# Optimization experiments

Measured on AMD Instinct MI355X. Metric: run time of the kernel, lower is better.

Reference implementation:

```python
import jax, jax.numpy as jnp
import numpy as np

# ---- static config (matches init_kwargs) ----
N0, N1 = 150000, 75000          # al nodes, test nodes
E = 200000                       # edges per edge type
D = 128                          # dim_h
L = 3                            # n_layers
T = 4                            # netypes
NAL = 50000                      # n_al vocab
NC = 3                           # n_classes
T_SRCS = [0, 0, 1, 1]
T_TGTS = [0, 1, 0, 1]
NODE_COUNTS = [N0, N1]


def setup_inputs() -> dict:
    key = jax.random.key(0)
    ks = jax.random.split(key, 16)
    x0_ids = jax.random.randint(ks[0], (N0,), 0, NAL, dtype=jnp.int32)
    x1_ids = jnp.zeros((N1,), dtype=jnp.int32)  # emb_test has a single row

    def make_edges(k, n_src, n_dst):
        k1, k2 = jax.random.split(k)
        src = jax.random.randint(k1, (E,), 0, n_src, dtype=jnp.int32)
        dst = jax.random.randint(k2, (E,), 0, n_dst, dtype=jnp.int32)
        return jnp.stack([src, dst])  # [2, E]

    es = [make_edges(ks[1 + j], NODE_COUNTS[T_SRCS[j]], NODE_COUNTS[T_TGTS[j]])
          for j in range(T)]

    s = 1.0 / np.sqrt(D)
    enc_al_w   = jax.random.normal(ks[5],  (NAL, D), jnp.float32) * s
    emb_test_w = jax.random.normal(ks[6],  (1, D),   jnp.float32) * s
    W_tgt = jax.random.normal(ks[7],  (L, T, D, D), jnp.float32) * s
    b_tgt = jax.random.normal(ks[8],  (L, T, D),    jnp.float32) * 0.01
    W_src = jax.random.normal(ks[9],  (L, T, D, D), jnp.float32) * s
    b_src = jax.random.normal(ks[10], (L, T, D),    jnp.float32) * 0.01
    emb_self = jax.random.normal(ks[11], (L, T, 2, D), jnp.float32) * s
    W_dec = jax.random.normal(ks[12], (NC, D), jnp.float32) * s
    b_dec = jax.random.normal(ks[13], (NC,),   jnp.float32) * 0.01
    return {
        "x0_ids": x0_ids, "x1_ids": x1_ids,
        "es0": es[0], "es1": es[1], "es2": es[2], "es3": es[3],
        "enc_al_w": enc_al_w, "emb_test_w": emb_test_w,
        "W_tgt": W_tgt, "b_tgt": b_tgt, "W_src": W_src, "b_src": b_src,
        "emb_self": emb_self, "W_dec": W_dec, "b_dec": b_dec,
    }


def reference(x0_ids, x1_ids, es0, es1, es2, es3,
              enc_al_w, emb_test_w, W_tgt, b_tgt, W_src, b_src,
              emb_self, W_dec, b_dec):
    ess = [es0, es1, es2, es3]
    # node-type embeddings
    xs = [enc_al_w[x0_ids], emb_test_w[x1_ids]]  # [N0,D], [N1,D]
    for i in range(L):
        out = [jnp.zeros((N0, D), xs[0].dtype), jnp.zeros((N1, D), xs[1].dtype)]
        for j in range(T):
            ts, tt = T_SRCS[j], T_TGTS[j]
            src, dst = ess[j][0], ess[j][1]
            # project node features first (same math as projecting gathered edges)
            h_src = xs[ts] @ W_src[i, j].T + b_src[i, j]   # lin_src(x_src)
            h_dst = xs[tt] @ W_tgt[i, j].T + b_tgt[i, j]   # lin_tgt(x_dst)
            self_flag = (dst == src).astype(jnp.int32)
            msg = h_dst[dst] + h_src[src] + emb_self[i, j][self_flag]  # [E,D]
            agg = jax.ops.segment_max(msg, dst, num_segments=NODE_COUNTS[tt])
            out[tt] = out[tt] + jax.nn.relu(agg)  # MPNN.forward applies relu
        xs = [jax.nn.relu(out[0]), jax.nn.relu(out[1])]
    last = xs[0] @ W_dec.T + b_dec                 # [N0, NC]
    return (last, jax.nn.softmax(last, axis=1))
```

## Files before the change

kernel.cpp:

```cpp
#include <hip/hip_runtime.h>
#include <hip/hip_bf16.h>

#define N0 150000
#define N1 75000
#define EE 200000
#define NAL 50000
#define NSEG (N0 + N1)
#define NSEG2 (2 * NSEG)
#define TOTE (4 * EE)

typedef unsigned short u16;
using s16x8 = __attribute__((ext_vector_type(8))) short;
using f32x4 = __attribute__((ext_vector_type(4))) float;
using u16x8 = __attribute__((ext_vector_type(8))) unsigned short;

__device__ __forceinline__ u16 f2b(float f) {
  unsigned int b = __float_as_uint(f);
  b += 0x7FFFu + ((b >> 16) & 1u);
  return (u16)(b >> 16);
}
__device__ __forceinline__ float b2f(u16 u) {
  return __uint_as_float(((unsigned int)u) << 16);
}

__global__ void sentinel_k(float* out, float val) {
  if (threadIdx.x == 0 && blockIdx.x == 0) out[0] = val;
}

__global__ __launch_bounds__(256) void prep_w(const float* __restrict__ Ws,
                                              const float* __restrict__ Wt,
                                              u16* __restrict__ BP) {
  int idx = blockIdx.x * 256 + threadIdx.x;
  int mk = idx & 16383;
  int slot = (idx >> 14) & 7;
  int i = idx >> 17;
  const int ssel[8] = {1, 0, 0, 1, 1, 1, 0, 0};
  const int sj[8]   = {0, 0, 2, 1, 2, 3, 1, 3};
  const float* W = ssel[slot] ? Ws : Wt;
  BP[idx] = f2b(W[(size_t)(i * 4 + sj[slot]) * 16384 + mk]);
}

__global__ __launch_bounds__(256) void embed_k(const int* __restrict__ ids,
                                               const float* __restrict__ tab,
                                               u16* __restrict__ X, int N, unsigned vocab) {
  int idx = blockIdx.x * 256 + threadIdx.x;
  int v = idx >> 4;
  if (v >= N) return;
  int q = (idx & 15) << 3;
  unsigned id = (unsigned)ids[v];
  if (id >= vocab) id = 0;
  const float* src = tab + (size_t)id * 128 + q;
  f32x4 x0 = *(const f32x4*)src;
  f32x4 x1 = *(const f32x4*)(src + 4);
  u16x8 o;
#pragma unroll
  for (int k = 0; k < 4; ++k) { o[k] = f2b(x0[k]); o[4 + k] = f2b(x1[k]); }
  *(u16x8*)(X + (size_t)v * 128 + q) = o;
}

__global__ __launch_bounds__(256) void count_all(const int* __restrict__ e0,
                                                 const int* __restrict__ e1,
                                                 const int* __restrict__ e2,
                                                 const int* __restrict__ e3,
                                                 int* __restrict__ cnt) {
  int i = blockIdx.x * 256 + threadIdx.x;
  if (i >= TOTE) return;
  int j = i / EE, r = i - j * EE;
  const int* es = (j == 0) ? e0 : (j == 1) ? e1 : (j == 2) ? e2 : e3;
  int dst = es[EE + r];
  int seg = (j & 1) ? N0 + dst : dst;
  atomicAdd(cnt + seg * 2 + (j >> 1), 1);
}

__global__ __launch_bounds__(512) void scan1_k(const int* __restrict__ cnt,
                                               int* __restrict__ off,
                                               int* __restrict__ part, int N) {
  __shared__ int sh[512];
  int t = threadIdx.x, i = blockIdx.x * 512 + t;
  int v = (i < N) ? cnt[i] : 0;
  sh[t] = v; __syncthreads();
  for (int s = 1; s < 512; s <<= 1) {
    int x = (t >= s) ? sh[t - s] : 0; __syncthreads();
    sh[t] += x; __syncthreads();
  }
  if (i < N) off[i] = sh[t] - v;
  if (t == 511) part[blockIdx.x] = sh[511];
}

__global__ __launch_bounds__(1024) void scan2_k(int* __restrict__ part, int n) {
  __shared__ int sh[1024];
  int t = threadIdx.x;
  int v = (t < n) ? part[t] : 0;
  sh[t] = v; __syncthreads();
  for (int s = 1; s < 1024; s <<= 1) {
    int x = (t >= s) ? sh[t - s] : 0; __syncthreads();
    sh[t] += x; __syncthreads();
  }
  if (t < n) part[t] = sh[t] - v;
}

__global__ __launch_bounds__(256) void scan3_k(int* __restrict__ off,
                                               const int* __restrict__ part, int N, int tot) {
  int i = blockIdx.x * 256 + threadIdx.x;
  if (i < N) off[i] += part[i >> 9];
  if (i == 0) off[N] = tot;
}

__global__ __launch_bounds__(256) void fill_all(const int* __restrict__ e0,
                                                const int* __restrict__ e1,
                                                const int* __restrict__ e2,
                                                const int* __restrict__ e3,
                                                const int* __restrict__ off,
                                                int* __restrict__ cur,
                                                int* __restrict__ einfo) {
  int i = blockIdx.x * 256 + threadIdx.x;
  if (i >= TOTE) return;
  int j = i / EE, r = i - j * EE;
  const int* es = (j == 0) ? e0 : (j == 1) ? e1 : (j == 2) ? e2 : e3;
  int src = es[r], dst = es[EE + r];
  int seg2 = ((j & 1) ? N0 + dst : dst) * 2 + (j >> 1);
  int pos = off[seg2] + atomicAdd(cur + seg2, 1);
  einfo[pos] = src | ((src == dst) ? (int)0x80000000 : 0);
}

__global__ __launch_bounds__(256, 5) void gemm_multi(const u16* __restrict__ A, int M,
                                                     const u16* __restrict__ W, int nw,
                                                     u16* __restrict__ C0,
                                                     u16* __restrict__ C1,
                                                     u16* __restrict__ C2,
                                                     u16* __restrict__ C3) {
  __shared__ u16 Al[64 * 128];
  __shared__ u16 Bl[64 * 128];
  const int t = threadIdx.x;
  const int row0 = blockIdx.x * 64;

#pragma unroll
  for (int u = 0; u < 4; ++u) {
    int c = u * 256 + t;
    int r = c >> 4, ch = c & 15;
    int rc = (row0 + r < M) ? (row0 + r) : (M - 1);
    int sw = ch ^ (r & 7);
    *(u16x8*)&Al[r * 128 + sw * 8] = *(const u16x8*)(A + (size_t)rc * 128 + ch * 8);
  }

  const int w = t >> 6, lane = t & 63;
  const int lr = lane & 15, g = lane >> 4;
  const int arow = (w * 16 + lr) * 128;

  u16x8 breg[4];
#pragma unroll
  for (int u = 0; u < 4; ++u) {
    int c = u * 256 + t;
    int r = c >> 4, ch = c & 15;
    breg[u] = *(const u16x8*)(W + r * 128 + ch * 8);
  }

  for (int ws = 0; ws < nw; ++ws) {
    u16* Cw = (ws == 0) ? C0 : (ws == 1) ? C1 : (ws == 2) ? C2 : C3;
#pragma unroll
    for (int h = 0; h < 2; ++h) {
      __builtin_amdgcn_sched_barrier(0);
      __builtin_amdgcn_s_barrier();
      __builtin_amdgcn_sched_barrier(0);

#pragma unroll
      for (int u = 0; u < 4; ++u) {
        int c = u * 256 + t;
        int r = c >> 4, ch = c & 15;
        int sw = ch ^ (r & 7);
        *(u16x8*)&Bl[r * 128 + sw * 8] = breg[u];
      }
      int nws = ws, nh = h + 1;
      if (nh == 2) { nh = 0; ++nws; }
      if (nws < nw) {
        const u16* Bn = W + (size_t)nws * 16384 + (size_t)nh * (64 * 128);
#pragma unroll
        for (int u = 0; u < 4; ++u) {
          int c = u * 256 + t;
          int r = c >> 4, ch = c & 15;
          breg[u] = *(const u16x8*)(Bn + r * 128 + ch * 8);
        }
      }
      asm volatile("s_waitcnt lgkmcnt(0)" ::: "memory");
      __builtin_amdgcn_sched_barrier(0);
      __builtin_amdgcn_s_barrier();
      __builtin_amdgcn_sched_barrier(0);

      f32x4 acc[4];
#pragma unroll
      for (int nf = 0; nf < 4; ++nf) acc[nf] = f32x4{0.f, 0.f, 0.f, 0.f};

#pragma unroll
      for (int ks = 0; ks < 4; ++ks) {
        int swz = ((ks * 4 + g) ^ (lr & 7)) * 8;
        s16x8 a = *(const s16x8*)&Al[arow + swz];
#pragma unroll
        for (int nf = 0; nf < 4; ++nf) {
          s16x8 b = *(const s16x8*)&Bl[(nf * 16 + lr) * 128 + swz];
          acc[nf] = __builtin_amdgcn_mfma_f32_16x16x32_bf16(a, b, acc[nf], 0, 0, 0);
        }
      }

#pragma unroll
      for (int nf = 0; nf < 4; ++nf) {
        int col = h * 64 + nf * 16 + lr;
#pragma unroll
        for (int j = 0; j < 4; ++j) {
          int orow = row0 + w * 16 + g * 4 + j;
          if (orow < M) Cw[(size_t)orow * 128 + col] = f2b(acc[nf][j]);
        }
      }
    }
  }
}

__global__ __launch_bounds__(256) void agg2_k(const int* __restrict__ off2,
                                              const int* __restrict__ einfo,
                                              int segbase,
                                              const u16* __restrict__ HSA,
                                              const u16* __restrict__ HSB,
                                              const u16* __restrict__ HD0,
                                              const u16* __restrict__ HD1,
                                              const float* __restrict__ bs0,
                                              const float* __restrict__ bt0,
                                              const float* __restrict__ bs1,
                                              const float* __restrict__ bt1,
                                              const float* __restrict__ esf0,
                                              const float* __restrict__ esf1,
                                              u16* __restrict__ Y, int N) {
  int idx = blockIdx.x * 256 + threadIdx.x;
  int d = idx >> 4;
  if (d >= N) return;
  int f8 = (idx & 15) << 3;
  int base = (segbase + d) * 2;
  int e0 = off2[base], e1 = off2[base + 1], e2 = off2[base + 2];

  float en[8], es_[8];
#pragma unroll
  for (int k = 0; k < 8; ++k) { en[k] = esf0[f8 + k]; es_[k] = esf0[128 + f8 + k]; }
  float m0[8];
#pragma unroll
  for (int k = 0; k < 8; ++k) m0[k] = -INFINITY;
  for (int e = e0; e < e1; ++e) {
    int info = einfo[e];
    int s = info & 0x7fffffff;
    bool self = (info < 0);
    u16x8 hv = *(const u16x8*)(HSA + (size_t)s * 128 + f8);
#pragma unroll
    for (int k = 0; k < 8; ++k)
      m0[k] = fmaxf(m0[k], b2f(hv[k]) + (self ? es_[k] : en[k]));
  }

#pragma unroll
  for (int k = 0; k < 8; ++k) { en[k] = esf1[f8 + k]; es_[k] = esf1[128 + f8 + k]; }
  float m1[8];
#pragma unroll
  for (int k = 0; k < 8; ++k) m1[k] = -INFINITY;
  for (int e = e1; e < e2; ++e) {
    int info = einfo[e];
    int s = info & 0x7fffffff;
    bool self = (info < 0);
    u16x8 hv = *(const u16x8*)(HSB + (size_t)s * 128 + f8);
#pragma unroll
    for (int k = 0; k < 8; ++k)
      m1[k] = fmaxf(m1[k], b2f(hv[k]) + (self ? es_[k] : en[k]));
  }

  u16x8 hd0 = *(const u16x8*)(HD0 + (size_t)d * 128 + f8);
  u16x8 hd1 = *(const u16x8*)(HD1 + (size_t)d * 128 + f8);
  u16x8 o;
#pragma unroll
  for (int k = 0; k < 8; ++k) {
    float r0 = fmaxf(b2f(hd0[k]) + bs0[f8 + k] + bt0[f8 + k] + m0[k], 0.f);
    float r1 = fmaxf(b2f(hd1[k]) + bs1[f8 + k] + bt1[f8 + k] + m1[k], 0.f);
    o[k] = f2b(r0 + r1);
  }
  *(u16x8*)(Y + (size_t)d * 128 + f8) = o;
}

__global__ __launch_bounds__(256) void decoder_k(const u16* __restrict__ X,
                                                 const float* __restrict__ Wd,
                                                 const float* __restrict__ bd,
                                                 float* __restrict__ out) {
  int v = blockIdx.x * 256 + threadIdx.x;
  if (v >= N0) return;
  float a0 = bd[0], a1 = bd[1], a2 = bd[2];
  const u16* x = X + (size_t)v * 128;
#pragma unroll
  for (int k = 0; k < 128; k += 8) {
    u16x8 xv = *(const u16x8*)(x + k);
#pragma unroll
    for (int u = 0; u < 8; ++u) {
      float xf = b2f(xv[u]);
      a0 = fmaf(xf, Wd[k + u], a0);
      a1 = fmaf(xf, Wd[128 + k + u], a1);
      a2 = fmaf(xf, Wd[256 + k + u], a2);
    }
  }
  float mx = fmaxf(a0, fmaxf(a1, a2));
  float e0 = expf(a0 - mx), e1 = expf(a1 - mx), e2 = expf(a2 - mx);
  float inv = 1.f / (e0 + e1 + e2);
  size_t b = (size_t)v * 3;
  out[b + 0] = a0; out[b + 1] = a1; out[b + 2] = a2;
  size_t b2 = (size_t)N0 * 3 + b;
  out[b2 + 0] = e0 * inv; out[b2 + 1] = e1 * inv; out[b2 + 2] = e2 * inv;
}

extern "C" void kernel_launch(void* const* d_in, const int* in_sizes, int n_in,
                              void* d_out, int out_size, void* d_ws, size_t ws_size,
                              hipStream_t stream) {
  float* out = (float*)d_out;

  const int expect[15] = {N0, N1, 2 * EE, 2 * EE, 2 * EE, 2 * EE,
                          NAL * 128, 128, 196608, 1536, 196608, 1536,
                          3072, 384, 3};
  bool ok = (n_in == 15);
  if (ok) for (int i = 0; i < 15; ++i) ok = ok && (in_sizes[i] == expect[i]);
  if (!ok) { sentinel_k<<<1, 64, 0, stream>>>(out, 500.f); return; }

  const int* x0_ids = (const int*)d_in[0];
  const int* x1_ids = (const int*)d_in[1];
  const int* es0 = (const int*)d_in[2];
  const int* es1 = (const int*)d_in[3];
  const int* es2 = (const int*)d_in[4];
  const int* es3 = (const int*)d_in[5];
  const float* enc_al   = (const float*)d_in[6];
  const float* emb_test = (const float*)d_in[7];
  const float* W_tgt    = (const float*)d_in[8];
  const float* b_tgt    = (const float*)d_in[9];
  const float* W_src    = (const float*)d_in[10];
  const float* b_src    = (const float*)d_in[11];
  const float* emb_self = (const float*)d_in[12];
  const float* W_dec    = (const float*)d_in[13];
  const float* b_dec    = (const float*)d_in[14];

  char* base = (char*)d_ws;
  size_t pos = 0;
  auto alloc = [&](size_t bytes) -> void* {
    void* r = base + pos;
    pos += (bytes + 255) & ~(size_t)255;
    return r;
  };
  u16* xs0 = (u16*)alloc((size_t)N0 * 128 * 2);
  u16* xs1 = (u16*)alloc((size_t)N1 * 128 * 2);
  u16* P0  = (u16*)alloc((size_t)N0 * 128 * 2);
  u16* P1  = (u16*)alloc((size_t)N0 * 128 * 2);
  u16* P2  = (u16*)alloc((size_t)N0 * 128 * 2);
  u16* P3  = (u16*)alloc((size_t)N1 * 128 * 2);
  u16* P4  = (u16*)alloc((size_t)N0 * 128 * 2);
  u16* BP  = (u16*)alloc((size_t)3 * 8 * 16384 * 2);
  int* off2   = (int*)alloc((size_t)(NSEG2 + 1) * 4);
  int* einfo  = (int*)alloc((size_t)TOTE * 4);
  int* counts = (int*)alloc((size_t)NSEG2 * 4);
  int* cursor = counts;
  int* part   = (int*)alloc(1024 * 4);
  if (pos > ws_size) { sentinel_k<<<1, 64, 0, stream>>>(out, 900.f); return; }

  prep_w<<<1536, 256, 0, stream>>>(W_src, W_tgt, BP);
  embed_k<<<(N0 * 16 + 255) / 256, 256, 0, stream>>>(x0_ids, enc_al, xs0, N0, NAL);
  embed_k<<<(N1 * 16 + 255) / 256, 256, 0, stream>>>(x1_ids, emb_test, xs1, N1, 1);

  const int EG = (TOTE + 255) / 256;
  const int nb = (NSEG2 + 511) / 512;
  hipMemsetAsync(counts, 0, (size_t)NSEG2 * 4, stream);
  count_all<<<EG, 256, 0, stream>>>(es0, es1, es2, es3, counts);
  scan1_k<<<nb, 512, 0, stream>>>(counts, off2, part, NSEG2);
  scan2_k<<<1, 1024, 0, stream>>>(part, nb);
  scan3_k<<<(NSEG2 + 255) / 256, 256, 0, stream>>>(off2, part, NSEG2, TOTE);
  hipMemsetAsync(cursor, 0, (size_t)NSEG2 * 4, stream);
  fill_all<<<EG, 256, 0, stream>>>(es0, es1, es2, es3, off2, cursor, einfo);

  const int G0 = (N0 + 63) / 64, G1 = (N1 + 63) / 64;
  const int GA0 = (N0 * 16 + 255) / 256, GA1 = (N1 * 16 + 255) / 256;
  for (int i = 0; i < 3; ++i) {
    const u16* BPi = BP + (size_t)i * 8 * 16384;
    gemm_multi<<<G0, 256, 0, stream>>>(xs0, N0, BPi + 0 * 16384, (i < 2) ? 4 : 3,
                                       P0, P1, P2, P4);
    gemm_multi<<<G1, 256, 0, stream>>>(xs1, N1, BPi + 4 * 16384, 1, P3, P3, P3, P3);
    agg2_k<<<GA0, 256, 0, stream>>>(off2, einfo, 0, P0, P3, P1, P2,
                                    b_src + (size_t)(i * 4 + 0) * 128, b_tgt + (size_t)(i * 4 + 0) * 128,
                                    b_src + (size_t)(i * 4 + 2) * 128, b_tgt + (size_t)(i * 4 + 2) * 128,
                                    emb_self + (size_t)(i * 4 + 0) * 256,
                                    emb_self + (size_t)(i * 4 + 2) * 256, xs0, N0);
    if (i < 2) {
      gemm_multi<<<G1, 256, 0, stream>>>(xs1, N1, BPi + 5 * 16384, 3, P3, P1, P2, P2);
      agg2_k<<<GA1, 256, 0, stream>>>(off2, einfo, N0, P4, P3, P1, P2,
                                      b_src + (size_t)(i * 4 + 1) * 128, b_tgt + (size_t)(i * 4 + 1) * 128,
                                      b_src + (size_t)(i * 4 + 3) * 128, b_tgt + (size_t)(i * 4 + 3) * 128,
                                      emb_self + (size_t)(i * 4 + 1) * 256,
                                      emb_self + (size_t)(i * 4 + 3) * 256, xs1, N1);
    }
  }

  decoder_k<<<(N0 + 255) / 256, 256, 0, stream>>>(xs0, W_dec, b_dec, out);
}
```

Before: 523.3 us.

## Fuse target-side projection GEMM into the max-aggregation kernel via LDS

Adds a gemm_agg kernel. Each block computes the two target-side projections for its 64 destination rows with MFMA, keeps them in shared memory, then runs the segment-max aggregation over those rows and writes the layer output. This removes the global writes and re-reads of two full projection buffers per node type per layer, and one launch. The weight slots are reordered so source projections come first, and the buffer set shrinks to match. The cost is that each thread now handles four destinations one after another, and the larger shared-memory footprint limits blocks per CU, so fewer irregular gathers are in flight to hide latency.

```diff
diff --git a/kernel.cpp b/kernel.cpp
--- a/kernel.cpp
+++ b/kernel.cpp
@@ -34,8 +34,8 @@
   int mk = idx & 16383;
   int slot = (idx >> 14) & 7;
   int i = idx >> 17;
-  const int ssel[8] = {1, 0, 0, 1, 1, 1, 0, 0};
-  const int sj[8]   = {0, 0, 2, 1, 2, 3, 1, 3};
+  const int ssel[8] = {1, 1, 1, 1, 0, 0, 0, 0};
+  const int sj[8]   = {0, 1, 2, 3, 0, 2, 1, 3};
   const float* W = ssel[slot] ? Ws : Wt;
   BP[idx] = f2b(W[(size_t)(i * 4 + sj[slot]) * 16384 + mk]);
 }
@@ -162,7 +162,6 @@
       __builtin_amdgcn_sched_barrier(0);
       __builtin_amdgcn_s_barrier();
       __builtin_amdgcn_sched_barrier(0);
-
 #pragma unroll
       for (int u = 0; u < 4; ++u) {
         int c = u * 256 + t;
@@ -189,7 +188,6 @@
       f32x4 acc[4];
 #pragma unroll
       for (int nf = 0; nf < 4; ++nf) acc[nf] = f32x4{0.f, 0.f, 0.f, 0.f};
-
 #pragma unroll
       for (int ks = 0; ks < 4; ++ks) {
         int swz = ((ks * 4 + g) ^ (lr & 7)) * 8;
@@ -200,7 +198,6 @@
           acc[nf] = __builtin_amdgcn_mfma_f32_16x16x32_bf16(a, b, acc[nf], 0, 0, 0);
         }
       }
-
 #pragma unroll
       for (int nf = 0; nf < 4; ++nf) {
         int col = h * 64 + nf * 16 + lr;
@@ -214,68 +211,147 @@
   }
 }
 
-__global__ __launch_bounds__(256) void agg2_k(const int* __restrict__ off2,
-                                              const int* __restrict__ einfo,
-                                              int segbase,
-                                              const u16* __restrict__ HSA,
-                                              const u16* __restrict__ HSB,
-                                              const u16* __restrict__ HD0,
-                                              const u16* __restrict__ HD1,
-                                              const float* __restrict__ bs0,
-                                              const float* __restrict__ bt0,
-                                              const float* __restrict__ bs1,
-                                              const float* __restrict__ bt1,
-                                              const float* __restrict__ esf0,
-                                              const float* __restrict__ esf1,
-                                              u16* __restrict__ Y, int N) {
-  int idx = blockIdx.x * 256 + threadIdx.x;
-  int d = idx >> 4;
-  if (d >= N) return;
-  int f8 = (idx & 15) << 3;
-  int base = (segbase + d) * 2;
-  int e0 = off2[base], e1 = off2[base + 1], e2 = off2[base + 2];
-
-  float en[8], es_[8];
-#pragma unroll
-  for (int k = 0; k < 8; ++k) { en[k] = esf0[f8 + k]; es_[k] = esf0[128 + f8 + k]; }
-  float m0[8];
-#pragma unroll
-  for (int k = 0; k < 8; ++k) m0[k] = -INFINITY;
-  for (int e = e0; e < e1; ++e) {
-    int info = einfo[e];
-    int s = info & 0x7fffffff;
-    bool self = (info < 0);
-    u16x8 hv = *(const u16x8*)(HSA + (size_t)s * 128 + f8);
-#pragma unroll
-    for (int k = 0; k < 8; ++k)
-      m0[k] = fmaxf(m0[k], b2f(hv[k]) + (self ? es_[k] : en[k]));
-  }
-
-#pragma unroll
-  for (int k = 0; k < 8; ++k) { en[k] = esf1[f8 + k]; es_[k] = esf1[128 + f8 + k]; }
-  float m1[8];
-#pragma unroll
-  for (int k = 0; k < 8; ++k) m1[k] = -INFINITY;
-  for (int e = e1; e < e2; ++e) {
-    int info = einfo[e];
-    int s = info & 0x7fffffff;
-    bool self = (info < 0);
-    u16x8 hv = *(const u16x8*)(HSB + (size_t)s * 128 + f8);
-#pragma unroll
-    for (int k = 0; k < 8; ++k)
-      m1[k] = fmaxf(m1[k], b2f(hv[k]) + (self ? es_[k] : en[k]));
-  }
-
-  u16x8 hd0 = *(const u16x8*)(HD0 + (size_t)d * 128 + f8);
-  u16x8 hd1 = *(const u16x8*)(HD1 + (size_t)d * 128 + f8);
-  u16x8 o;
-#pragma unroll
-  for (int k = 0; k < 8; ++k) {
-    float r0 = fmaxf(b2f(hd0[k]) + bs0[f8 + k] + bt0[f8 + k] + m0[k], 0.f);
-    float r1 = fmaxf(b2f(hd1[k]) + bs1[f8 + k] + bt1[f8 + k] + m1[k], 0.f);
-    o[k] = f2b(r0 + r1);
-  }
-  *(u16x8*)(Y + (size_t)d * 128 + f8) = o;
+#define HDS 264
+__global__ __launch_bounds__(256, 3) void gemm_agg(const u16* __restrict__ A,
+                                                   const u16* __restrict__ W2,
+                                                   const int* __restrict__ off2,
+                                                   const int* __restrict__ einfo,
+                                                   int segbase,
+                                                   const u16* __restrict__ HSA,
+                                                   const u16* __restrict__ HSB,
+                                                   const float* __restrict__ bs0,
+                                                   const float* __restrict__ bt0,
+                                                   const float* __restrict__ bs1,
+                                                   const float* __restrict__ bt1,
+                                                   const float* __restrict__ esf0,
+                                                   const float* __restrict__ esf1,
+                                                   u16* __restrict__ Y, int N) {
+  __shared__ u16 Bl[64 * 128];
+  __shared__ u16 HDl[64 * HDS];
+  const int t = threadIdx.x;
+  const int row0 = blockIdx.x * 64;
+  const int w = t >> 6, lane = t & 63;
+  const int lr = lane & 15, g = lane >> 4;
+
+  int arow = row0 + w * 16 + lr;
+  int arc = (arow < N) ? arow : (N - 1);
+  const u16* Ab = A + (size_t)arc * 128 + g * 8;
+  u16x8 a[4];
+#pragma unroll
+  for (int ks = 0; ks < 4; ++ks) a[ks] = *(const u16x8*)(Ab + ks * 32);
+
+  u16x8 breg[4];
+#pragma unroll
+  for (int u = 0; u < 4; ++u) {
+    int c = u * 256 + t;
+    int r = c >> 4, ch = c & 15;
+    breg[u] = *(const u16x8*)(W2 + r * 128 + ch * 8);
+  }
+
+#pragma unroll
+  for (int ws = 0; ws < 2; ++ws) {
+#pragma unroll
+    for (int h = 0; h < 2; ++h) {
+      __builtin_amdgcn_sched_barrier(0);
+      __builtin_amdgcn_s_barrier();
+      __builtin_amdgcn_sched_barrier(0);
+#pragma unroll
+      for (int u = 0; u < 4; ++u) {
+        int c = u * 256 + t;
+        int r = c >> 4, ch = c & 15;
+        int sw = ch ^ (r & 7);
+        *(u16x8*)&Bl[r * 128 + sw * 8] = breg[u];
+      }
+      int nws = ws, nh = h + 1;
+      if (nh == 2) { nh = 0; ++nws; }
+      if (nws < 2) {
+        const u16* Bn = W2 + (size_t)nws * 16384 + (size_t)nh * (64 * 128);
+#pragma unroll
+        for (int u = 0; u < 4; ++u) {
+          int c = u * 256 + t;
+          int r = c >> 4, ch = c & 15;
+          breg[u] = *(const u16x8*)(Bn + r * 128 + ch * 8);
+        }
+      }
+      asm volatile("s_waitcnt lgkmcnt(0)" ::: "memory");
+      __builtin_amdgcn_sched_barrier(0);
+      __builtin_amdgcn_s_barrier();
+      __builtin_amdgcn_sched_barrier(0);
+
+      f32x4 acc[4];
+#pragma unroll
+      for (int nf = 0; nf < 4; ++nf) acc[nf] = f32x4{0.f, 0.f, 0.f, 0.f};
+#pragma unroll
+      for (int ks = 0; ks < 4; ++ks) {
+        int swz = ((ks * 4 + g) ^ (lr & 7)) * 8;
+#pragma unroll
+        for (int nf = 0; nf < 4; ++nf) {
+          s16x8 b = *(const s16x8*)&Bl[(nf * 16 + lr) * 128 + swz];
+          acc[nf] = __builtin_amdgcn_mfma_f32_16x16x32_bf16((s16x8)a[ks], b, acc[nf], 0, 0, 0);
+        }
+      }
+#pragma unroll
+      for (int nf = 0; nf < 4; ++nf) {
+        int col = ws * 128 + h * 64 + nf * 16 + lr;
+#pragma unroll
+        for (int j = 0; j < 4; ++j)
+          HDl[(w * 16 + g * 4 + j) * HDS + col] = f2b(acc[nf][j]);
+      }
+    }
+  }
+  __syncthreads();
+
+#pragma unroll 1
+  for (int sw = 0; sw < 4; ++sw) {
+    int dl = sw * 16 + (t >> 4);
+    int d = row0 + dl;
+    if (d >= N) continue;
+    int f8 = (t & 15) << 3;
+    int base = (segbase + d) * 2;
+    int e0 = off2[base], e1 = off2[base + 1], e2 = off2[base + 2];
+
+    float en[8], es_[8];
+#pragma unroll
+    for (int k = 0; k < 8; ++k) { en[k] = esf0[f8 + k]; es_[k] = esf0[128 + f8 + k]; }
+    float m0[8];
+#pragma unroll
+    for (int k = 0; k < 8; ++k) m0[k] = -INFINITY;
+    for (int e = e0; e < e1; ++e) {
+      int info = einfo[e];
+      int s = info & 0x7fffffff;
+      bool self = (info < 0);
+      u16x8 hv = *(const u16x8*)(HSA + (size_t)s * 128 + f8);
+#pragma unroll
+      for (int k = 0; k < 8; ++k)
+        m0[k] = fmaxf(m0[k], b2f(hv[k]) + (self ? es_[k] : en[k]));
+    }
+
+#pragma unroll
+    for (int k = 0; k < 8; ++k) { en[k] = esf1[f8 + k]; es_[k] = esf1[128 + f8 + k]; }
+    float m1[8];
+#pragma unroll
+    for (int k = 0; k < 8; ++k) m1[k] = -INFINITY;
+    for (int e = e1; e < e2; ++e) {
+      int info = einfo[e];
+      int s = info & 0x7fffffff;
+      bool self = (info < 0);
+      u16x8 hv = *(const u16x8*)(HSB + (size_t)s * 128 + f8);
+#pragma unroll
+      for (int k = 0; k < 8; ++k)
+        m1[k] = fmaxf(m1[k], b2f(hv[k]) + (self ? es_[k] : en[k]));
+    }
+
+    u16x8 hd0 = *(const u16x8*)&HDl[dl * HDS + f8];
+    u16x8 hd1 = *(const u16x8*)&HDl[dl * HDS + 128 + f8];
+    u16x8 o;
+#pragma unroll
+    for (int k = 0; k < 8; ++k) {
+      float r0 = fmaxf(b2f(hd0[k]) + bs0[f8 + k] + bt0[f8 + k] + m0[k], 0.f);
+      float r1 = fmaxf(b2f(hd1[k]) + bs1[f8 + k] + bt1[f8 + k] + m1[k], 0.f);
+      o[k] = f2b(r0 + r1);
+    }
+    *(u16x8*)(Y + (size_t)d * 128 + f8) = o;
+  }
 }
 
 __global__ __launch_bounds__(256) void decoder_k(const u16* __restrict__ X,
@@ -344,10 +420,9 @@
   u16* xs0 = (u16*)alloc((size_t)N0 * 128 * 2);
   u16* xs1 = (u16*)alloc((size_t)N1 * 128 * 2);
   u16* P0  = (u16*)alloc((size_t)N0 * 128 * 2);
-  u16* P1  = (u16*)alloc((size_t)N0 * 128 * 2);
-  u16* P2  = (u16*)alloc((size_t)N0 * 128 * 2);
+  u16* P4  = (u16*)alloc((size_t)N0 * 128 * 2);
   u16* P3  = (u16*)alloc((size_t)N1 * 128 * 2);
-  u16* P4  = (u16*)alloc((size_t)N0 * 128 * 2);
+  u16* P5  = (u16*)alloc((size_t)N1 * 128 * 2);
   u16* BP  = (u16*)alloc((size_t)3 * 8 * 16384 * 2);
   int* off2   = (int*)alloc((size_t)(NSEG2 + 1) * 4);
   int* einfo  = (int*)alloc((size_t)TOTE * 4);
@@ -371,24 +446,22 @@
   fill_all<<<EG, 256, 0, stream>>>(es0, es1, es2, es3, off2, cursor, einfo);
 
   const int G0 = (N0 + 63) / 64, G1 = (N1 + 63) / 64;
-  const int GA0 = (N0 * 16 + 255) / 256, GA1 = (N1 * 16 + 255) / 256;
   for (int i = 0; i < 3; ++i) {
     const u16* BPi = BP + (size_t)i * 8 * 16384;
-    gemm_multi<<<G0, 256, 0, stream>>>(xs0, N0, BPi + 0 * 16384, (i < 2) ? 4 : 3,
-                                       P0, P1, P2, P4);
-    gemm_multi<<<G1, 256, 0, stream>>>(xs1, N1, BPi + 4 * 16384, 1, P3, P3, P3, P3);
-    agg2_k<<<GA0, 256, 0, stream>>>(off2, einfo, 0, P0, P3, P1, P2,
-                                    b_src + (size_t)(i * 4 + 0) * 128, b_tgt + (size_t)(i * 4 + 0) * 128,
-                                    b_src + (size_t)(i * 4 + 2) * 128, b_tgt + (size_t)(i * 4 + 2) * 128,
-                                    emb_self + (size_t)(i * 4 + 0) * 256,
-                                    emb_self + (size_t)(i * 4 + 2) * 256, xs0, N0);
+    const int nws = (i < 2) ? 2 : 1;
+    gemm_multi<<<G0, 256, 0, stream>>>(xs0, N0, BPi + 0 * 16384, nws, P0, P4, P4, P4);
+    gemm_multi<<<G1, 256, 0, stream>>>(xs1, N1, BPi + 2 * 16384, nws, P3, P5, P5, P5);
+    gemm_agg<<<G0, 256, 0, stream>>>(xs0, BPi + 4 * 16384, off2, einfo, 0, P0, P3,
+                                     b_src + (size_t)(i * 4 + 0) * 128, b_tgt + (size_t)(i * 4 + 0) * 128,
+                                     b_src + (size_t)(i * 4 + 2) * 128, b_tgt + (size_t)(i * 4 + 2) * 128,
+                                     emb_self + (size_t)(i * 4 + 0) * 256,
+                                     emb_self + (size_t)(i * 4 + 2) * 256, xs0, N0);
     if (i < 2) {
-      gemm_multi<<<G1, 256, 0, stream>>>(xs1, N1, BPi + 5 * 16384, 3, P3, P1, P2, P2);
-      agg2_k<<<GA1, 256, 0, stream>>>(off2, einfo, N0, P4, P3, P1, P2,
-                                      b_src + (size_t)(i * 4 + 1) * 128, b_tgt + (size_t)(i * 4 + 1) * 128,
-                                      b_src + (size_t)(i * 4 + 3) * 128, b_tgt + (size_t)(i * 4 + 3) * 128,
-                                      emb_self + (size_t)(i * 4 + 1) * 256,
-                                      emb_self + (size_t)(i * 4 + 3) * 256, xs1, N1);
+      gemm_agg<<<G1, 256, 0, stream>>>(xs1, BPi + 6 * 16384, off2, einfo, N0, P4, P5,
+                                       b_src + (size_t)(i * 4 + 1) * 128, b_tgt + (size_t)(i * 4 + 1) * 128,
+                                       b_src + (size_t)(i * 4 + 3) * 128, b_tgt + (size_t)(i * 4 + 3) * 128,
+                                       emb_self + (size_t)(i * 4 + 1) * 256,
+                                       emb_self + (size_t)(i * 4 + 3) * 256, xs1, N1);
     }
   }
 
```

Result: slower. 665.2 us (+27.1%).
